# Kernel optimization log

Measured on AMD Instinct MI355X. Metric: run time of the kernel, lower is better.

Reference implementation:

```python
import jax, jax.numpy as jnp
import numpy as np

B, S, G, E, NI = 128, 40000, 4000, 16, 4
H1, H2 = 1024, 256
EPS = 1e-5


def _ln(x, w, b):
    m = x.mean(-1, keepdims=True)
    v = ((x - m) ** 2).mean(-1, keepdims=True)
    return (x - m) / jnp.sqrt(v + EPS) * w + b


def setup_inputs() -> dict:
    key = jax.random.key(0)
    ks = jax.random.split(key, 20)
    x = jax.random.normal(ks[0], (B, S), dtype=jnp.float32)
    impact_indices = jax.random.randint(ks[1], (S,), 0, NI)
    # fixed SNP->gene mask: each SNP connects to exactly one gene
    gene_of_snp = jax.random.randint(ks[2], (S,), 0, G)
    mask = jnp.zeros((G, S), jnp.float32).at[gene_of_snp, jnp.arange(S)].set(1.0)
    # impact attention params
    emb = 0.02 * jax.random.normal(ks[3], (NI, E))
    proj_w = jax.random.normal(ks[4], (E, E)) * np.sqrt(2.0 / (E + E))
    proj_b = jnp.zeros((E,))
    ln_i_w, ln_i_b = jnp.ones((E,)), jnp.zeros((E,))
    scale_w = 0.005 * jax.random.normal(ks[5], (1, E)); scale_b = jnp.zeros((1,))
    bias_w = 0.005 * jax.random.normal(ks[6], (1, E)); bias_b = jnp.zeros((1,))
    # masked linear: per-row std = sqrt(1/fan_in) (gelu path)
    fan_in = jnp.clip(mask.sum(1), 1.0, None)  # [G]
    mw = jax.random.normal(ks[7], (G, S)) * jnp.sqrt(1.0 / fan_in)[:, None]
    mb = jnp.zeros((G,))
    ln1_w, ln1_b = jnp.ones((G,)), jnp.zeros((G,))
    fc1_w = jax.random.normal(ks[8], (H1, G)) * np.sqrt(2.0 / G); fc1_b = jnp.zeros((H1,))
    lnA_w, lnA_b = jnp.ones((H1,)), jnp.zeros((H1,))
    fc2_w = jax.random.normal(ks[9], (H2, H1)) * np.sqrt(2.0 / H1); fc2_b = jnp.zeros((H2,))
    lnB_w, lnB_b = jnp.ones((H2,)), jnp.zeros((H2,))
    out_w = jax.random.normal(ks[10], (1, H2)) * np.sqrt(2.0 / (H2 + 1)); out_b = jnp.zeros((1,))
    return dict(x=x, impact_indices=impact_indices, mask=mask, emb=emb,
                proj_w=proj_w, proj_b=proj_b, ln_i_w=ln_i_w, ln_i_b=ln_i_b,
                scale_w=scale_w, scale_b=scale_b, bias_w=bias_w, bias_b=bias_b,
                mw=mw, mb=mb, ln1_w=ln1_w, ln1_b=ln1_b,
                fc1_w=fc1_w, fc1_b=fc1_b, lnA_w=lnA_w, lnA_b=lnA_b,
                fc2_w=fc2_w, fc2_b=fc2_b, lnB_w=lnB_w, lnB_b=lnB_b,
                out_w=out_w, out_b=out_b)


def reference(x, impact_indices, mask, emb, proj_w, proj_b, ln_i_w, ln_i_b,
              scale_w, scale_b, bias_w, bias_b, mw, mb, ln1_w, ln1_b,
              fc1_w, fc1_b, lnA_w, lnA_b, fc2_w, fc2_b, lnB_w, lnB_b,
              out_w, out_b):
    gelu = lambda t: jax.nn.gelu(t, approximate=False)
    # SNP impact attention
    h = emb[impact_indices]                       # [S,E]
    h = h @ proj_w.T + proj_b
    h = gelu(_ln(h, ln_i_w, ln_i_b))
    scale = (h @ scale_w.T + scale_b)[:, 0]       # [S]
    bias = (h @ bias_w.T + bias_b)[:, 0]          # [S]
    attn = 2.0 * jax.nn.sigmoid(x * scale + bias) # [B,S]
    xs = x * attn
    # masked linear SNP -> gene
    g = xs @ (mw * mask).T + mb                   # [B,G]
    g = gelu(_ln(g, ln1_w, ln1_b))
    # dense MLP head
    y = gelu(_ln(g @ fc1_w.T + fc1_b, lnA_w, lnA_b))
    y = gelu(_ln(y @ fc2_w.T + fc2_b, lnB_w, lnB_b))
    return y @ out_w.T + out_b                    # [B,1]
```

## Files before the change

kernel.cpp:

```cpp
#include <hip/hip_runtime.h>
#include <hip/hip_bf16.h>

#define S_  40000
#define G_  4000
#define B_  128
#define NI_ 4
#define E_  16
#define H1_ 1024
#define H2_ 256
#define EPSF 1e-5f
#define KSPLIT 10
#define MAXH 128
#define DET_BLOCKS 2048
#define NWAVES (DET_BLOCKS * 4)
#define NCHUNK 78125

typedef unsigned uvec4 __attribute__((ext_vector_type(4)));

#define OFF_STATS ((size_t)64)
#define OFF_XST   ((size_t)1024)
#define OFF_GT    (OFF_XST + (size_t)S_ * B_)
#define OFF_Y1P   (OFF_GT  + (size_t)G_ * B_)
#define OFF_CNT   (OFF_Y1P + (size_t)KSPLIT * B_ * H1_)
#define OFF_HITS  (OFF_CNT + (size_t)4096)

__device__ __forceinline__ float gelu_f(float x) {
    return 0.5f * x * (1.0f + erff(x * 0.70710678118654752f));
}

__global__ __launch_bounds__(256) void kAttn(
        const float* __restrict__ x, const int* __restrict__ ii,
        const float* __restrict__ emb, const float* __restrict__ proj_w,
        const float* __restrict__ proj_b, const float* __restrict__ ln_i_w,
        const float* __restrict__ ln_i_b, const float* __restrict__ scale_w,
        const float* __restrict__ scale_b, const float* __restrict__ bias_w,
        const float* __restrict__ bias_b,
        float* __restrict__ xs_t, int* __restrict__ cnt, float* __restrict__ stats) {
    const int tid = threadIdx.x;
    if (blockIdx.x == 625) {
        for (int i = tid; i < G_; i += 256) cnt[i] = 0;
        if (tid < 256) stats[tid] = 0.f;
        return;
    }
    __shared__ float tile[64][129];
    __shared__ float hs[NI_][E_];
    __shared__ float tab[8];
    if (tid < 64) {
        const int iv = tid >> 4, e = tid & 15;
        float s = proj_b[e];
        for (int f = 0; f < E_; ++f) s += emb[iv * E_ + f] * proj_w[e * E_ + f];
        hs[iv][e] = s;
    }
    __syncthreads();
    if (tid < NI_) {
        float m = 0.f;
        for (int e = 0; e < E_; ++e) m += hs[tid][e];
        m *= (1.f / E_);
        float v = 0.f;
        for (int e = 0; e < E_; ++e) { float d = hs[tid][e] - m; v += d * d; }
        v *= (1.f / E_);
        const float r = 1.f / sqrtf(v + EPSF);
        float sc = scale_b[0], bi = bias_b[0];
        for (int e = 0; e < E_; ++e) {
            float t = (hs[tid][e] - m) * r * ln_i_w[e] + ln_i_b[e];
            t = gelu_f(t);
            sc += t * scale_w[e];
            bi += t * bias_w[e];
        }
        tab[tid] = sc;
        tab[4 + tid] = bi;
    }
    __syncthreads();
    const int s0 = blockIdx.x * 64;
    const int ls = tid & 63;
    const int bg = tid >> 6;
    const int s  = s0 + ls;
    const int iv = ii[s];
    const float sc = tab[iv];
    const float bi = tab[4 + iv];
#pragma unroll
    for (int j = 0; j < 32; ++j) {
        int b = bg + j * 4;
        float xv = x[(size_t)b * S_ + s];
        float at = 2.f / (1.f + expf(-(xv * sc + bi)));
        tile[ls][b] = xv * at;
    }
    __syncthreads();
    const int b2 = tid & 127;
    const int lg = tid >> 7;
#pragma unroll
    for (int j = 0; j < 32; ++j) {
        int l = lg + j * 2;
        xs_t[(size_t)(s0 + l) * B_ + b2] = tile[l][b2];
    }
}

__global__ __launch_bounds__(256) void kDetect(const float* __restrict__ mask,
                                               int* __restrict__ cnt,
                                               int* __restrict__ hits) {
    const int lane = threadIdx.x & 63;
    const int gw   = blockIdx.x * 4 + (threadIdx.x >> 6);
    const uvec4* __restrict__ m4 = (const uvec4*)mask;
    for (int c = gw; c < NCHUNK; c += NWAVES) {
        const int base = c * 512;
        uvec4 v[8];
#pragma unroll
        for (int u = 0; u < 8; ++u)
            v[u] = __builtin_nontemporal_load(&m4[base + u * 64 + lane]);
        unsigned or8 = 0, or4[8];
#pragma unroll
        for (int u = 0; u < 8; ++u) {
            or4[u] = v[u].x | v[u].y | v[u].z | v[u].w;
            or8 |= or4[u];
        }
        if (__any(or8 != 0)) {
#pragma unroll
            for (int u = 0; u < 8; ++u) {
                if (or4[u]) {
                    const int f0 = (base + u * 64 + lane) * 4;
                    if (v[u].x) { int row = (f0 + 0) / S_; int sl = atomicAdd(&cnt[row], 1); if (sl < MAXH) hits[row * MAXH + sl] = (f0 + 0) - row * S_; }
                    if (v[u].y) { int row = (f0 + 1) / S_; int sl = atomicAdd(&cnt[row], 1); if (sl < MAXH) hits[row * MAXH + sl] = (f0 + 1) - row * S_; }
                    if (v[u].z) { int row = (f0 + 2) / S_; int sl = atomicAdd(&cnt[row], 1); if (sl < MAXH) hits[row * MAXH + sl] = (f0 + 2) - row * S_; }
                    if (v[u].w) { int row = (f0 + 3) / S_; int sl = atomicAdd(&cnt[row], 1); if (sl < MAXH) hits[row * MAXH + sl] = (f0 + 3) - row * S_; }
                }
            }
        }
    }
}

__global__ __launch_bounds__(256) void kB(const int* __restrict__ cnt,
                                          const int* __restrict__ hits,
                                          const float* __restrict__ mw,
                                          const float* __restrict__ mb,
                                          const float* __restrict__ xs_t,
                                          float* __restrict__ g_t) {
    const int lane = threadIdx.x & 63;
    const int wv   = threadIdx.x >> 6;
    const int rowbase = blockIdx.x * 8 + wv * 2;
#pragma unroll
    for (int rr = 0; rr < 2; ++rr) {
        const int row = rowbase + rr;
        const int n = min(cnt[row], MAXH);
        float a0 = 0.f, a1 = 0.f;
        for (int j = 0; j < n; ++j) {
            const int s = hits[row * MAXH + j];
            const float w = mw[(size_t)row * S_ + s];
            a0 += w * xs_t[(size_t)s * B_ + lane];
            a1 += w * xs_t[(size_t)s * B_ + 64 + lane];
        }
        const float bias = mb[row];
        g_t[(size_t)row * B_ + lane]      = a0 + bias;
        g_t[(size_t)row * B_ + 64 + lane] = a1 + bias;
    }
}

__global__ __launch_bounds__(256) void k4_stats(const float* __restrict__ g_t,
                                                float* __restrict__ stats) {
    const int b = threadIdx.x & 127;
    const int h = threadIdx.x >> 7;
    const int g0 = blockIdx.x * 32;
    float s = 0.f, q = 0.f;
#pragma unroll
    for (int r = h; r < 32; r += 2) {
        float v = g_t[(size_t)(g0 + r) * B_ + b];
        s += v; q += v * v;
    }
    atomicAdd(&stats[b], s);
    atomicAdd(&stats[128 + b], q);
}

__global__ __launch_bounds__(256) void k6_fc1(const float* __restrict__ g_t,
                                              const float* __restrict__ stats,
                                              const float* __restrict__ ln1_w,
                                              const float* __restrict__ ln1_b,
                                              const float* __restrict__ fc1_w,
                                              float* __restrict__ y1p) {
    __shared__ float As[16 * 128];
    __shared__ float Ws[16][64];
    __shared__ float Sm[128];
    __shared__ float Sr[128];
    const int tid  = threadIdx.x;
    const int lane = tid & 63;
    const int wv   = tid >> 6;
    const int h0   = blockIdx.x * 64;
    const int k0   = blockIdx.y * 400;
    const int hh   = wv * 16;
    if (tid < 128) {
        float sm = stats[tid] * (1.f / G_);
        float var = stats[128 + tid] * (1.f / G_) - sm * sm;
        Sm[tid] = sm;
        Sr[tid] = 1.f / sqrtf(var + EPSF);
    }
    float acc0[16], acc1[16];
#pragma unroll
    for (int j = 0; j < 16; ++j) { acc0[j] = 0.f; acc1[j] = 0.f; }
    __syncthreads();
    for (int ch = 0; ch < 25; ++ch) {
        const int kc = k0 + ch * 16;
        __syncthreads();
        {
#pragma unroll
            for (int half = 0; half < 2; ++half) {
                const int idx = tid * 4 + half * 1024;
                const int kk = idx >> 7, b0 = idx & 127;
                float4 g4 = *(const float4*)(g_t + (size_t)(kc + kk) * B_ + b0);
                float4 m4 = *(const float4*)(&Sm[b0]);
                float4 r4 = *(const float4*)(&Sr[b0]);
                const float w = ln1_w[kc + kk], bb = ln1_b[kc + kk];
                float4 o;
                o.x = gelu_f((g4.x - m4.x) * r4.x * w + bb);
                o.y = gelu_f((g4.y - m4.y) * r4.y * w + bb);
                o.z = gelu_f((g4.z - m4.z) * r4.z * w + bb);
                o.w = gelu_f((g4.w - m4.w) * r4.w * w + bb);
                *(float4*)(&As[idx]) = o;
            }
        }
        {
            const int h = tid & 63, q = tid >> 6;
            float4 w4 = *(const float4*)(fc1_w + (size_t)(h0 + h) * G_ + kc + q * 4);
            Ws[q * 4 + 0][h] = w4.x; Ws[q * 4 + 1][h] = w4.y;
            Ws[q * 4 + 2][h] = w4.z; Ws[q * 4 + 3][h] = w4.w;
        }
        __syncthreads();
#pragma unroll
        for (int k = 0; k < 16; ++k) {
            const float a0  = As[k * 128 + lane];
            const float a1v = As[k * 128 + 64 + lane];
            const float4* wrow = (const float4*)(&Ws[k][hh]);
#pragma unroll
            for (int jq = 0; jq < 4; ++jq) {
                float4 w4 = wrow[jq];
                acc0[jq * 4 + 0] += a0 * w4.x;  acc1[jq * 4 + 0] += a1v * w4.x;
                acc0[jq * 4 + 1] += a0 * w4.y;  acc1[jq * 4 + 1] += a1v * w4.y;
                acc0[jq * 4 + 2] += a0 * w4.z;  acc1[jq * 4 + 2] += a1v * w4.z;
                acc0[jq * 4 + 3] += a0 * w4.w;  acc1[jq * 4 + 3] += a1v * w4.w;
            }
        }
    }
    float* out0 = y1p + ((size_t)blockIdx.y * B_ + lane) * H1_ + h0 + hh;
    float* out1 = out0 + (size_t)64 * H1_;
    float4* o0 = (float4*)out0;
    float4* o1 = (float4*)out1;
#pragma unroll
    for (int q = 0; q < 4; ++q) {
        o0[q] = make_float4(acc0[q*4+0], acc0[q*4+1], acc0[q*4+2], acc0[q*4+3]);
        o1[q] = make_float4(acc1[q*4+0], acc1[q*4+1], acc1[q*4+2], acc1[q*4+3]);
    }
}

__global__ __launch_bounds__(256) void k78_head(const float* __restrict__ y1p,
                                                const float* __restrict__ fc1_b,
                                                const float* __restrict__ lnA_w,
                                                const float* __restrict__ lnA_b,
                                                const float* __restrict__ fc2_w,
                                                const float* __restrict__ fc2_b,
                                                const float* __restrict__ lnB_w,
                                                const float* __restrict__ lnB_b,
                                                const float* __restrict__ out_w,
                                                const float* __restrict__ out_b,
                                                float* __restrict__ out) {
    const int b = blockIdx.x, tid = threadIdx.x, lane = tid & 63, wv = tid >> 6;
    __shared__ float a_s[H1_];
    __shared__ float y_s[H2_];
    __shared__ float red[8];
    float v[4];
    float s_ = 0.f, q_ = 0.f;
#pragma unroll
    for (int j = 0; j < 4; ++j) {
        int h = tid + j * 256;
        float s = fc1_b[h];
#pragma unroll
        for (int ks = 0; ks < KSPLIT; ++ks)
            s += y1p[(size_t)ks * B_ * H1_ + (size_t)b * H1_ + h];
        v[j] = s; s_ += s; q_ += s * s;
    }
    for (int off = 32; off; off >>= 1) { s_ += __shfl_down(s_, off); q_ += __shfl_down(q_, off); }
    if (lane == 0) { red[wv] = s_; red[4 + wv] = q_; }
    __syncthreads();
    {
        float Ssum = red[0] + red[1] + red[2] + red[3];
        float Qsum = red[4] + red[5] + red[6] + red[7];
        float m = Ssum / 1024.f, var = Qsum / 1024.f - m * m;
        float r = 1.f / sqrtf(var + EPSF);
#pragma unroll
        for (int j = 0; j < 4; ++j) {
            int h = tid + j * 256;
            a_s[h] = gelu_f((v[j] - m) * r * lnA_w[h] + lnA_b[h]);
        }
    }
    __syncthreads();
    for (int oi = 0; oi < 64; ++oi) {
        int o = wv * 64 + oi;
        const float4* wr = (const float4*)(fc2_w + (size_t)o * H1_);
        float d = 0.f;
#pragma unroll
        for (int q = 0; q < 4; ++q) {
            float4 ww = wr[lane + 64 * q];
            float4 aa = ((const float4*)a_s)[lane + 64 * q];
            d += aa.x * ww.x + aa.y * ww.y + aa.z * ww.z + aa.w * ww.w;
        }
        for (int off = 32; off; off >>= 1) d += __shfl_down(d, off);
        if (lane == 0) y_s[o] = d + fc2_b[o];
    }
    __syncthreads();
    float yv = y_s[tid];
    float s2 = yv, q2 = yv * yv;
    for (int off = 32; off; off >>= 1) { s2 += __shfl_down(s2, off); q2 += __shfl_down(q2, off); }
    __syncthreads();
    if (lane == 0) { red[wv] = s2; red[4 + wv] = q2; }
    __syncthreads();
    float Ssum = red[0] + red[1] + red[2] + red[3];
    float Qsum = red[4] + red[5] + red[6] + red[7];
    float m = Ssum / (float)H2_, var = Qsum / (float)H2_ - m * m;
    float r = 1.f / sqrtf(var + EPSF);
    float val = gelu_f((yv - m) * r * lnB_w[tid] + lnB_b[tid]) * out_w[tid];
    __syncthreads();
    float t_ = val;
    for (int off = 32; off; off >>= 1) t_ += __shfl_down(t_, off);
    if (lane == 0) red[wv] = t_;
    __syncthreads();
    if (tid == 0)
        out[b] = red[0] + red[1] + red[2] + red[3] + out_b[0];
}

extern "C" void kernel_launch(void* const* d_in, const int* in_sizes, int n_in,
                              void* d_out, int out_size, void* d_ws, size_t ws_size,
                              hipStream_t stream) {
    const float* x       = (const float*)d_in[0];
    const int*   ii      = (const int*)  d_in[1];
    const float* mask    = (const float*)d_in[2];
    const float* emb     = (const float*)d_in[3];
    const float* proj_w  = (const float*)d_in[4];
    const float* proj_b  = (const float*)d_in[5];
    const float* ln_i_w  = (const float*)d_in[6];
    const float* ln_i_b  = (const float*)d_in[7];
    const float* scale_w = (const float*)d_in[8];
    const float* scale_b = (const float*)d_in[9];
    const float* bias_w  = (const float*)d_in[10];
    const float* bias_b  = (const float*)d_in[11];
    const float* mw      = (const float*)d_in[12];
    const float* mb      = (const float*)d_in[13];
    const float* ln1_w   = (const float*)d_in[14];
    const float* ln1_b   = (const float*)d_in[15];
    const float* fc1_w   = (const float*)d_in[16];
    const float* fc1_b   = (const float*)d_in[17];
    const float* lnA_w   = (const float*)d_in[18];
    const float* lnA_b   = (const float*)d_in[19];
    const float* fc2_w   = (const float*)d_in[20];
    const float* fc2_b   = (const float*)d_in[21];
    const float* lnB_w   = (const float*)d_in[22];
    const float* lnB_b   = (const float*)d_in[23];
    const float* out_w   = (const float*)d_in[24];
    const float* out_b   = (const float*)d_in[25];

    float* ws    = (float*)d_ws;
    float* stats = ws + OFF_STATS;
    float* xs_t  = ws + OFF_XST;
    float* g_t   = ws + OFF_GT;
    float* y1p   = ws + OFF_Y1P;
    int*   cnt   = (int*)(ws + OFF_CNT);
    int*   hits  = (int*)(ws + OFF_HITS);
    float* out   = (float*)d_out;

    hipLaunchKernelGGL(kAttn, dim3(626), dim3(256), 0, stream,
                       x, ii, emb, proj_w, proj_b, ln_i_w, ln_i_b, scale_w, scale_b,
                       bias_w, bias_b, xs_t, cnt, stats);
    hipLaunchKernelGGL(kDetect, dim3(DET_BLOCKS), dim3(256), 0, stream, mask, cnt, hits);
    hipLaunchKernelGGL(kB, dim3(G_ / 8), dim3(256), 0, stream, cnt, hits, mw, mb, xs_t, g_t);
    hipLaunchKernelGGL(k4_stats, dim3(125), dim3(256), 0, stream, g_t, stats);
    hipLaunchKernelGGL(k6_fc1, dim3(H1_ / 64, KSPLIT), dim3(256), 0, stream,
                       g_t, stats, ln1_w, ln1_b, fc1_w, y1p);
    hipLaunchKernelGGL(k78_head, dim3(B_), dim3(256), 0, stream,
                       y1p, fc1_b, lnA_w, lnA_b, fc2_w, fc2_b, lnB_w, lnB_b, out_w, out_b, out);
}
```

Baseline: 269.0 us.

## Fuse attention and mask-detect kernels, fold LN stats into kB, widen fc1 split

Result: no change. 271.8 us (+1.0%).

```diff
diff --git a/kernel.cpp b/kernel.cpp
--- a/kernel.cpp
+++ b/kernel.cpp
@@ -9,10 +9,11 @@
 #define H1_ 1024
 #define H2_ 256
 #define EPSF 1e-5f
-#define KSPLIT 10
+#define KSPLIT 50
 #define MAXH 128
-#define DET_BLOCKS 2048
-#define NWAVES (DET_BLOCKS * 4)
+#define ATT_B 128
+#define DET_B 2048
+#define NTILE 625
 #define NCHUNK 78125
 
 typedef unsigned uvec4 __attribute__((ext_vector_type(4)));
@@ -28,23 +29,53 @@
     return 0.5f * x * (1.0f + erff(x * 0.70710678118654752f));
 }
 
-__global__ __launch_bounds__(256) void kAttn(
+__global__ __launch_bounds__(256) void kFused(
         const float* __restrict__ x, const int* __restrict__ ii,
         const float* __restrict__ emb, const float* __restrict__ proj_w,
         const float* __restrict__ proj_b, const float* __restrict__ ln_i_w,
         const float* __restrict__ ln_i_b, const float* __restrict__ scale_w,
         const float* __restrict__ scale_b, const float* __restrict__ bias_w,
-        const float* __restrict__ bias_b,
-        float* __restrict__ xs_t, int* __restrict__ cnt, float* __restrict__ stats) {
-    const int tid = threadIdx.x;
-    if (blockIdx.x == 625) {
-        for (int i = tid; i < G_; i += 256) cnt[i] = 0;
-        if (tid < 256) stats[tid] = 0.f;
+        const float* __restrict__ bias_b, const float* __restrict__ mask,
+        float* __restrict__ xs_t, int* __restrict__ cnt, int* __restrict__ hits,
+        float* __restrict__ stats) {
+    const int bid = blockIdx.x, tid = threadIdx.x;
+    const int lane = tid & 63, wv = tid >> 6;
+
+    if (bid >= ATT_B) {
+        const int gw = (bid - ATT_B) * 4 + wv;
+        const uvec4* __restrict__ m4 = (const uvec4*)mask;
+        for (int c = gw; c < NCHUNK; c += DET_B * 4) {
+            const int base = c * 512;
+            uvec4 v[8];
+#pragma unroll
+            for (int u = 0; u < 8; ++u)
+                v[u] = __builtin_nontemporal_load(&m4[base + u * 64 + lane]);
+            unsigned or8 = 0, or4[8];
+#pragma unroll
+            for (int u = 0; u < 8; ++u) {
+                or4[u] = v[u].x | v[u].y | v[u].z | v[u].w;
+                or8 |= or4[u];
+            }
+            if (__any(or8 != 0)) {
+#pragma unroll
+                for (int u = 0; u < 8; ++u) {
+                    if (or4[u]) {
+                        const int f0 = (base + u * 64 + lane) * 4;
+                        if (v[u].x) { int row = (f0 + 0) / S_; int sl = atomicAdd(&cnt[row], 1); if (sl < MAXH) hits[row * MAXH + sl] = (f0 + 0) - row * S_; }
+                        if (v[u].y) { int row = (f0 + 1) / S_; int sl = atomicAdd(&cnt[row], 1); if (sl < MAXH) hits[row * MAXH + sl] = (f0 + 1) - row * S_; }
+                        if (v[u].z) { int row = (f0 + 2) / S_; int sl = atomicAdd(&cnt[row], 1); if (sl < MAXH) hits[row * MAXH + sl] = (f0 + 2) - row * S_; }
+                        if (v[u].w) { int row = (f0 + 3) / S_; int sl = atomicAdd(&cnt[row], 1); if (sl < MAXH) hits[row * MAXH + sl] = (f0 + 3) - row * S_; }
+                    }
+                }
+            }
+        }
         return;
     }
+
     __shared__ float tile[64][129];
     __shared__ float hs[NI_][E_];
     __shared__ float tab[8];
+    if (bid == 0 && tid < 256) stats[tid] = 0.f;
     if (tid < 64) {
         const int iv = tid >> 4, e = tid & 15;
         float s = proj_b[e];
@@ -71,60 +102,28 @@
         tab[4 + tid] = bi;
     }
     __syncthreads();
-    const int s0 = blockIdx.x * 64;
-    const int ls = tid & 63;
-    const int bg = tid >> 6;
-    const int s  = s0 + ls;
-    const int iv = ii[s];
-    const float sc = tab[iv];
-    const float bi = tab[4 + iv];
-#pragma unroll
-    for (int j = 0; j < 32; ++j) {
-        int b = bg + j * 4;
-        float xv = x[(size_t)b * S_ + s];
-        float at = 2.f / (1.f + expf(-(xv * sc + bi)));
-        tile[ls][b] = xv * at;
-    }
-    __syncthreads();
-    const int b2 = tid & 127;
-    const int lg = tid >> 7;
-#pragma unroll
-    for (int j = 0; j < 32; ++j) {
-        int l = lg + j * 2;
-        xs_t[(size_t)(s0 + l) * B_ + b2] = tile[l][b2];
-    }
-}
-
-__global__ __launch_bounds__(256) void kDetect(const float* __restrict__ mask,
-                                               int* __restrict__ cnt,
-                                               int* __restrict__ hits) {
-    const int lane = threadIdx.x & 63;
-    const int gw   = blockIdx.x * 4 + (threadIdx.x >> 6);
-    const uvec4* __restrict__ m4 = (const uvec4*)mask;
-    for (int c = gw; c < NCHUNK; c += NWAVES) {
-        const int base = c * 512;
-        uvec4 v[8];
-#pragma unroll
-        for (int u = 0; u < 8; ++u)
-            v[u] = __builtin_nontemporal_load(&m4[base + u * 64 + lane]);
-        unsigned or8 = 0, or4[8];
-#pragma unroll
-        for (int u = 0; u < 8; ++u) {
-            or4[u] = v[u].x | v[u].y | v[u].z | v[u].w;
-            or8 |= or4[u];
-        }
-        if (__any(or8 != 0)) {
-#pragma unroll
-            for (int u = 0; u < 8; ++u) {
-                if (or4[u]) {
-                    const int f0 = (base + u * 64 + lane) * 4;
-                    if (v[u].x) { int row = (f0 + 0) / S_; int sl = atomicAdd(&cnt[row], 1); if (sl < MAXH) hits[row * MAXH + sl] = (f0 + 0) - row * S_; }
-                    if (v[u].y) { int row = (f0 + 1) / S_; int sl = atomicAdd(&cnt[row], 1); if (sl < MAXH) hits[row * MAXH + sl] = (f0 + 1) - row * S_; }
-                    if (v[u].z) { int row = (f0 + 2) / S_; int sl = atomicAdd(&cnt[row], 1); if (sl < MAXH) hits[row * MAXH + sl] = (f0 + 2) - row * S_; }
-                    if (v[u].w) { int row = (f0 + 3) / S_; int sl = atomicAdd(&cnt[row], 1); if (sl < MAXH) hits[row * MAXH + sl] = (f0 + 3) - row * S_; }
-                }
-            }
-        }
+    for (int t = bid; t < NTILE; t += ATT_B) {
+        const int s0 = t * 64;
+        const int s  = s0 + lane;
+        const int iv = ii[s];
+        const float sc = tab[iv];
+        const float bi = tab[4 + iv];
+#pragma unroll
+        for (int j = 0; j < 32; ++j) {
+            int b = wv + j * 4;
+            float xv = x[(size_t)b * S_ + s];
+            float at = 2.f / (1.f + expf(-(xv * sc + bi)));
+            tile[lane][b] = xv * at;
+        }
+        __syncthreads();
+        const int b2 = tid & 127;
+        const int lg = tid >> 7;
+#pragma unroll
+        for (int j = 0; j < 32; ++j) {
+            int l = lg + j * 2;
+            xs_t[(size_t)(s0 + l) * B_ + b2] = tile[l][b2];
+        }
+        __syncthreads();
     }
 }
 
@@ -133,7 +132,9 @@
                                           const float* __restrict__ mw,
                                           const float* __restrict__ mb,
                                           const float* __restrict__ xs_t,
-                                          float* __restrict__ g_t) {
+                                          float* __restrict__ g_t,
+                                          float* __restrict__ stats) {
+    __shared__ float rowacc[8][128];
     const int lane = threadIdx.x & 63;
     const int wv   = threadIdx.x >> 6;
     const int rowbase = blockIdx.x * 8 + wv * 2;
@@ -149,24 +150,21 @@
             a1 += w * xs_t[(size_t)s * B_ + 64 + lane];
         }
         const float bias = mb[row];
-        g_t[(size_t)row * B_ + lane]      = a0 + bias;
-        g_t[(size_t)row * B_ + 64 + lane] = a1 + bias;
-    }
-}
-
-__global__ __launch_bounds__(256) void k4_stats(const float* __restrict__ g_t,
-                                                float* __restrict__ stats) {
-    const int b = threadIdx.x & 127;
-    const int h = threadIdx.x >> 7;
-    const int g0 = blockIdx.x * 32;
-    float s = 0.f, q = 0.f;
-#pragma unroll
-    for (int r = h; r < 32; r += 2) {
-        float v = g_t[(size_t)(g0 + r) * B_ + b];
-        s += v; q += v * v;
-    }
-    atomicAdd(&stats[b], s);
-    atomicAdd(&stats[128 + b], q);
+        a0 += bias; a1 += bias;
+        g_t[(size_t)row * B_ + lane]      = a0;
+        g_t[(size_t)row * B_ + 64 + lane] = a1;
+        rowacc[wv * 2 + rr][lane]      = a0;
+        rowacc[wv * 2 + rr][64 + lane] = a1;
+    }
+    __syncthreads();
+    const int b = threadIdx.x & 127, half = threadIdx.x >> 7;
+    float acc = 0.f;
+#pragma unroll
+    for (int r = 0; r < 8; ++r) {
+        float v = rowacc[r][b];
+        acc += half ? v * v : v;
+    }
+    atomicAdd(&stats[half * 128 + b], acc);
 }
 
 __global__ __launch_bounds__(256) void k6_fc1(const float* __restrict__ g_t,
@@ -183,7 +181,8 @@
     const int lane = tid & 63;
     const int wv   = tid >> 6;
     const int h0   = blockIdx.x * 64;
-    const int k0   = blockIdx.y * 400;
+    const int kb   = blockIdx.y;
+    const int k0   = kb * 80;
     const int hh   = wv * 16;
     if (tid < 128) {
         float sm = stats[tid] * (1.f / G_);
@@ -195,7 +194,7 @@
 #pragma unroll
     for (int j = 0; j < 16; ++j) { acc0[j] = 0.f; acc1[j] = 0.f; }
     __syncthreads();
-    for (int ch = 0; ch < 25; ++ch) {
+    for (int ch = 0; ch < 5; ++ch) {
         const int kc = k0 + ch * 16;
         __syncthreads();
         {
@@ -237,7 +236,7 @@
             }
         }
     }
-    float* out0 = y1p + ((size_t)blockIdx.y * B_ + lane) * H1_ + h0 + hh;
+    float* out0 = y1p + ((size_t)kb * B_ + lane) * H1_ + h0 + hh;
     float* out1 = out0 + (size_t)64 * H1_;
     float4* o0 = (float4*)out0;
     float4* o1 = (float4*)out1;
@@ -269,9 +268,9 @@
     for (int j = 0; j < 4; ++j) {
         int h = tid + j * 256;
         float s = fc1_b[h];
-#pragma unroll
+#pragma unroll 10
         for (int ks = 0; ks < KSPLIT; ++ks)
-            s += y1p[(size_t)ks * B_ * H1_ + (size_t)b * H1_ + h];
+            s += y1p[((size_t)ks * B_ + b) * H1_ + h];
         v[j] = s; s_ += s; q_ += s * s;
     }
     for (int off = 32; off; off >>= 1) { s_ += __shfl_down(s_, off); q_ += __shfl_down(q_, off); }
@@ -362,13 +361,13 @@
     int*   hits  = (int*)(ws + OFF_HITS);
     float* out   = (float*)d_out;
 
-    hipLaunchKernelGGL(kAttn, dim3(626), dim3(256), 0, stream,
+    hipMemsetAsync(cnt, 0, G_ * sizeof(int), stream);
+    hipLaunchKernelGGL(kFused, dim3(ATT_B + DET_B), dim3(256), 0, stream,
                        x, ii, emb, proj_w, proj_b, ln_i_w, ln_i_b, scale_w, scale_b,
-                       bias_w, bias_b, xs_t, cnt, stats);
-    hipLaunchKernelGGL(kDetect, dim3(DET_BLOCKS), dim3(256), 0, stream, mask, cnt, hits);
-    hipLaunchKernelGGL(kB, dim3(G_ / 8), dim3(256), 0, stream, cnt, hits, mw, mb, xs_t, g_t);
-    hipLaunchKernelGGL(k4_stats, dim3(125), dim3(256), 0, stream, g_t, stats);
-    hipLaunchKernelGGL(k6_fc1, dim3(H1_ / 64, KSPLIT), dim3(256), 0, stream,
+                       bias_w, bias_b, mask, xs_t, cnt, hits, stats);
+    hipLaunchKernelGGL(kB, dim3(G_ / 8), dim3(256), 0, stream,
+                       cnt, hits, mw, mb, xs_t, g_t, stats);
+    hipLaunchKernelGGL(k6_fc1, dim3(16, KSPLIT), dim3(256), 0, stream,
                        g_t, stats, ln1_w, ln1_b, fc1_w, y1p);
     hipLaunchKernelGGL(k78_head, dim3(B_), dim3(256), 0, stream,
                        y1p, fc1_b, lnA_w, lnA_b, fc2_w, fc2_b, lnB_w, lnB_b, out_w, out_b, out);
```
